# Optimization experiments

Hardware: AMD Instinct MI355X
Metric: run time of the kernel (lower is better)

The kernel has to match this reference:

```python
import jax, jax.numpy as jnp
from jax import lax
import numpy as np

KERNEL_SIZE = 5
GROUP_SIZE = 40
GMAX = 160                      # g sampled in [0, GMAX)
MAX_ITERS = (GMAX - 1) // GROUP_SIZE   # static upper bound on |g|//group_size = 3
B = 4096
D = 8192


def _circ_conv(x, k):
    # x: [1, B, D], k: [B, K] -> grouped (depthwise) circular conv1d, groups=B
    pad = KERNEL_SIZE - 1
    left = pad // 2
    xp = jnp.pad(x, ((0, 0), (0, 0), (left, pad - left)), mode='wrap')
    return lax.conv_general_dilated(
        xp, k[:, None, :], window_strides=(1,), padding='VALID',
        feature_group_count=k.shape[0], dimension_numbers=('NCH', 'OIH', 'NCH'))


def setup_inputs() -> dict:
    key = jax.random.key(0)
    k1, k2, k3 = jax.random.split(key, 3)
    x = jax.random.normal(k1, (B, D), dtype=jnp.float32)
    g = jax.random.randint(k2, (B,), 0, GMAX, dtype=jnp.int32)
    kernels = jax.random.normal(k3, (2 * GROUP_SIZE + 1, KERNEL_SIZE), dtype=jnp.float32)
    return {"x": x, "g": g, "kernels": kernels}


def reference(x, g, kernels):
    G = GROUP_SIZE
    xc = x[None]                          # [1, B, D]  (x.view(-1,1,D).permute(1,0,2))
    sign = jnp.sign(g)                    # [B]
    iters = jnp.abs(g) // G               # [B] data-dependent per-sample loop count
    max_it = jnp.max(iters)               # dynamic max over the batch
    max_k = kernels[sign * G + G]         # [B, K]
    id_k = kernels[G]                     # [K] learned 'identity' kernel
    # true delta kernel: exact no-op under circular pad, used for steps past max_it
    delta = jnp.zeros((KERNEL_SIZE,), x.dtype).at[(KERNEL_SIZE - 1) // 2].set(1.0)

    h = xc
    for i in range(MAX_ITERS):            # static bound; delta makes extra steps no-ops
        inactive = jnp.where(i < max_it, id_k, delta)          # [K]
        k_i = jnp.where((i < iters)[:, None], max_k, inactive[None, :])  # [B, K]
        h = _circ_conv(h, k_i)
    rem = jnp.abs(g) % G
    fin_k = kernels[rem * sign + G]       # [B, K]
    out = _circ_conv(h, fin_k)            # [1, B, D]
    return jnp.transpose(out, (1, 0, 2))  # [B, 1, D]
```

## Files before the change

kernel.cpp:

```cpp
#include <hip/hip_runtime.h>

#define BB 4096
#define DD 8192
#define KK 5
#define GS 40
#define MAXIT 3
#define EFF 17
#define CHUNK 2048
#define C4 (CHUNK/4)
#define DF4 (DD/4)
#define EPAD 20
#define WS_OFF 64

typedef float vf4 __attribute__((ext_vector_type(4)));

__device__ __forceinline__ int iabs(int a) { return a < 0 ? -a : a; }

template<int LEN>
__device__ __forceinline__ void compose5(float* e, const float* k5) {
    float ne[LEN + KK - 1];
#pragma unroll
    for (int m = 0; m < LEN + KK - 1; ++m) ne[m] = 0.f;
#pragma unroll
    for (int m = 0; m < LEN; ++m)
#pragma unroll
        for (int j = 0; j < KK; ++j) ne[m + j] += e[m] * k5[j];
#pragma unroll
    for (int m = 0; m < LEN + KK - 1; ++m) e[m] = ne[m];
}

__device__ __forceinline__ void pick5(int i, int iters, int max_it,
                                      const float* maxk, const float* idk,
                                      float* k5) {
#pragma unroll
    for (int j = 0; j < KK; ++j)
        k5[j] = (i < iters) ? maxk[j]
              : ((i < max_it) ? idk[j] : ((j == (KK - 1) / 2) ? 1.f : 0.f));
}

__global__ __launch_bounds__(256) void k_compose(const int* __restrict__ g,
                                                 const float* __restrict__ kernels,
                                                 float* __restrict__ wsE) {
    __shared__ int red[256];
    const int t = threadIdx.x;

    const int4* g4 = (const int4*)g;
    int m = 0;
    for (int i = t; i < BB / 4; i += 256) {
        int4 v = g4[i];
        m = max(m, max(max(iabs(v.x), iabs(v.y)), max(iabs(v.z), iabs(v.w))));
    }
    red[t] = m;
    __syncthreads();
    for (int s = 128; s > 0; s >>= 1) {
        if (t < s) red[t] = max(red[t], red[t + s]);
        __syncthreads();
    }
    const int max_it = red[0] / GS;

    const int r  = blockIdx.x * 256 + t;
    const int gv = g[r];
    const int sign  = gv > 0 ? 1 : (gv < 0 ? -1 : 0);
    const int a     = iabs(gv);
    const int iters = a / GS;
    const int rem   = a % GS;

    const float* mk = kernels + (size_t)(sign * GS + GS) * KK;
    const float* ik = kernels + (size_t)GS * KK;
    const float* fk = kernels + (size_t)(rem * sign + GS) * KK;
    float maxk[KK], idk[KK], fink[KK];
#pragma unroll
    for (int j = 0; j < KK; ++j) { maxk[j] = mk[j]; idk[j] = ik[j]; fink[j] = fk[j]; }

    float e[EPAD];
#pragma unroll
    for (int q = 0; q < EPAD; ++q) e[q] = 0.f;
    e[0] = 1.f;

    float k5[KK];
    pick5(0, iters, max_it, maxk, idk, k5); compose5<1>(e, k5);
    pick5(1, iters, max_it, maxk, idk, k5); compose5<5>(e, k5);
    pick5(2, iters, max_it, maxk, idk, k5); compose5<9>(e, k5);
    compose5<13>(e, fink);

    vf4* dst = (vf4*)(wsE + (size_t)r * EPAD);
    vf4 o0; o0.x = e[0];  o0.y = e[1];  o0.z = e[2];  o0.w = e[3];
    vf4 o1; o1.x = e[4];  o1.y = e[5];  o1.z = e[6];  o1.w = e[7];
    vf4 o2; o2.x = e[8];  o2.y = e[9];  o2.z = e[10]; o2.w = e[11];
    vf4 o3; o3.x = e[12]; o3.y = e[13]; o3.z = e[14]; o3.w = e[15];
    vf4 o4; o4.x = e[16]; o4.y = e[17]; o4.z = e[18]; o4.w = e[19];
    dst[0] = o0; dst[1] = o1; dst[2] = o2; dst[3] = o3; dst[4] = o4;
}

__global__ __launch_bounds__(256) void k_conv_pre(const float* __restrict__ x,
                                                  const float* __restrict__ wsE,
                                                  float* __restrict__ out) {
    __shared__ float lds[CHUNK + 16];
    float4* ldsv = (float4*)lds;

    const int bi   = blockIdx.x;
    const int b    = bi >> 2;
    const int ch   = bi & 3;
    const int t    = threadIdx.x;
    const int c0f4 = ch * C4;

    const float4* xr = (const float4*)(x + (size_t)b * DD);

    ldsv[2 + t]       = xr[c0f4 + t];
    ldsv[2 + t + 256] = xr[c0f4 + t + 256];
    if (t == 0) {
        ldsv[0] = xr[(c0f4 - 2) & (DF4 - 1)];
        ldsv[1] = xr[(c0f4 - 1) & (DF4 - 1)];
    } else if (t == 1) {
        ldsv[514] = xr[(c0f4 + C4)     & (DF4 - 1)];
        ldsv[515] = xr[(c0f4 + C4 + 1) & (DF4 - 1)];
    }

    const float4* ev = (const float4*)(wsE + (size_t)b * EPAD);
    float4 e0 = ev[0], e1 = ev[1], e2 = ev[2], e3 = ev[3], e4 = ev[4];
    float e[EFF] = { e0.x, e0.y, e0.z, e0.w,
                     e1.x, e1.y, e1.z, e1.w,
                     e2.x, e2.y, e2.z, e2.w,
                     e3.x, e3.y, e3.z, e3.w,
                     e4.x };

    __syncthreads();

    vf4* outr = (vf4*)(out + (size_t)b * DD);
#pragma unroll
    for (int jb = 0; jb < 2; ++jb) {
        const int v = jb * 256 + t;
        float f[EFF + 3];
#pragma unroll
        for (int q = 0; q < 5; ++q) {
            float4 val = ldsv[v + q];
            f[q * 4 + 0] = val.x; f[q * 4 + 1] = val.y;
            f[q * 4 + 2] = val.z; f[q * 4 + 3] = val.w;
        }
        float oc[4];
#pragma unroll
        for (int c = 0; c < 4; ++c) {
            float s = 0.f;
#pragma unroll
            for (int m = 0; m < EFF; ++m) s += e[m] * f[c + m];
            oc[c] = s;
        }
        vf4 o;
        o.x = oc[0]; o.y = oc[1]; o.z = oc[2]; o.w = oc[3];
        __builtin_nontemporal_store(o, outr + c0f4 + v);
    }
}

__global__ __launch_bounds__(256) void k_max_it(const int* __restrict__ g,
                                                int* __restrict__ ws) {
    __shared__ int red[256];
    int t = threadIdx.x;
    int m = 0;
    for (int i = t; i < BB; i += 256) m = max(m, iabs(g[i]));
    red[t] = m;
    __syncthreads();
    for (int s = 128; s > 0; s >>= 1) {
        if (t < s) red[t] = max(red[t], red[t + s]);
        __syncthreads();
    }
    if (t == 0) ws[0] = red[0] / GS;
}

__global__ __launch_bounds__(256) void k_conv(const float* __restrict__ x,
                                              const int* __restrict__ g,
                                              const float* __restrict__ kernels,
                                              const int* __restrict__ ws,
                                              float* __restrict__ out) {
    __shared__ float lds[CHUNK + 16];
    float4* ldsv = (float4*)lds;

    const int bi   = blockIdx.x;
    const int b    = bi >> 2;
    const int ch   = bi & 3;
    const int t    = threadIdx.x;
    const int c0f4 = ch * C4;

    const float4* xr = (const float4*)(x + (size_t)b * DD);

    ldsv[2 + t]       = xr[c0f4 + t];
    ldsv[2 + t + 256] = xr[c0f4 + t + 256];
    if (t == 0) {
        ldsv[0] = xr[(c0f4 - 2) & (DF4 - 1)];
        ldsv[1] = xr[(c0f4 - 1) & (DF4 - 1)];
    } else if (t == 1) {
        ldsv[514] = xr[(c0f4 + C4)     & (DF4 - 1)];
        ldsv[515] = xr[(c0f4 + C4 + 1) & (DF4 - 1)];
    }

    const int gv    = g[b];
    const int sign  = gv > 0 ? 1 : (gv < 0 ? -1 : 0);
    const int a     = iabs(gv);
    const int iters = a / GS;
    const int rem   = a % GS;
    const int max_it = ws[0];

    float maxk[KK], idk[KK], fink[KK];
    const float* mk = kernels + (size_t)(sign * GS + GS) * KK;
    const float* ik = kernels + (size_t)GS * KK;
    const float* fk = kernels + (size_t)(rem * sign + GS) * KK;
#pragma unroll
    for (int j = 0; j < KK; ++j) { maxk[j] = mk[j]; idk[j] = ik[j]; fink[j] = fk[j]; }

    float e[EPAD];
#pragma unroll
    for (int q = 0; q < EPAD; ++q) e[q] = 0.f;
    e[0] = 1.f;
    float k5[KK];
    pick5(0, iters, max_it, maxk, idk, k5); compose5<1>(e, k5);
    pick5(1, iters, max_it, maxk, idk, k5); compose5<5>(e, k5);
    pick5(2, iters, max_it, maxk, idk, k5); compose5<9>(e, k5);
    compose5<13>(e, fink);

    __syncthreads();

    vf4* outr = (vf4*)(out + (size_t)b * DD);
#pragma unroll
    for (int jb = 0; jb < 2; ++jb) {
        const int v = jb * 256 + t;
        float f[EFF + 3];
#pragma unroll
        for (int q = 0; q < 5; ++q) {
            float4 val = ldsv[v + q];
            f[q * 4 + 0] = val.x; f[q * 4 + 1] = val.y;
            f[q * 4 + 2] = val.z; f[q * 4 + 3] = val.w;
        }
        float oc[4];
#pragma unroll
        for (int c = 0; c < 4; ++c) {
            float s = 0.f;
#pragma unroll
            for (int m = 0; m < EFF; ++m) s += e[m] * f[c + m];
            oc[c] = s;
        }
        vf4 o;
        o.x = oc[0]; o.y = oc[1]; o.z = oc[2]; o.w = oc[3];
        __builtin_nontemporal_store(o, outr + c0f4 + v);
    }
}

extern "C" void kernel_launch(void* const* d_in, const int* in_sizes, int n_in,
                              void* d_out, int out_size, void* d_ws, size_t ws_size,
                              hipStream_t stream) {
    const float* x       = (const float*)d_in[0];
    const int*   g       = (const int*)d_in[1];
    const float* kernels = (const float*)d_in[2];
    float*       out     = (float*)d_out;

    const size_t need = (size_t)(WS_OFF + BB * EPAD) * sizeof(float);
    if (ws_size >= need) {
        float* wsE = (float*)d_ws + WS_OFF;
        k_compose<<<BB / 256, 256, 0, stream>>>(g, kernels, wsE);
        k_conv_pre<<<BB * (DD / CHUNK), 256, 0, stream>>>(x, wsE, out);
    } else {
        int* ws = (int*)d_ws;
        k_max_it<<<1, 256, 0, stream>>>(g, ws);
        k_conv<<<BB * (DD / CHUNK), 256, 0, stream>>>(x, g, kernels, ws, out);
    }
}
```

Baseline: 235.8 us.

## Replace LDS-staged chunked conv with direct global float4 loads, one block per row

The LDS staging and __syncthreads are removed. Each thread now reads its five overlapping float4 neighbours straight from global memory, relying on the caches to absorb the 5x redundant reads. The grid changes from four chunks per row to one block per row, with each thread looping over 8 float4 outputs. Nontemporal stores become plain stores. This trades the LDS round-trip and barrier for more cache-served global loads, and changes grid occupancy and store caching behaviour.

```diff
diff --git a/kernel.cpp b/kernel.cpp
--- a/kernel.cpp
+++ b/kernel.cpp
@@ -6,8 +6,6 @@
 #define GS 40
 #define MAXIT 3
 #define EFF 17
-#define CHUNK 2048
-#define C4 (CHUNK/4)
 #define DF4 (DD/4)
 #define EPAD 20
 #define WS_OFF 64
@@ -92,29 +90,11 @@
     dst[0] = o0; dst[1] = o1; dst[2] = o2; dst[3] = o3; dst[4] = o4;
 }
 
-__global__ __launch_bounds__(256) void k_conv_pre(const float* __restrict__ x,
-                                                  const float* __restrict__ wsE,
-                                                  float* __restrict__ out) {
-    __shared__ float lds[CHUNK + 16];
-    float4* ldsv = (float4*)lds;
-
-    const int bi   = blockIdx.x;
-    const int b    = bi >> 2;
-    const int ch   = bi & 3;
-    const int t    = threadIdx.x;
-    const int c0f4 = ch * C4;
-
-    const float4* xr = (const float4*)(x + (size_t)b * DD);
-
-    ldsv[2 + t]       = xr[c0f4 + t];
-    ldsv[2 + t + 256] = xr[c0f4 + t + 256];
-    if (t == 0) {
-        ldsv[0] = xr[(c0f4 - 2) & (DF4 - 1)];
-        ldsv[1] = xr[(c0f4 - 1) & (DF4 - 1)];
-    } else if (t == 1) {
-        ldsv[514] = xr[(c0f4 + C4)     & (DF4 - 1)];
-        ldsv[515] = xr[(c0f4 + C4 + 1) & (DF4 - 1)];
-    }
+__global__ __launch_bounds__(256) void k_conv_direct(const float* __restrict__ x,
+                                                     const float* __restrict__ wsE,
+                                                     float* __restrict__ out) {
+    const int b = blockIdx.x;
+    const int t = threadIdx.x;
 
     const float4* ev = (const float4*)(wsE + (size_t)b * EPAD);
     float4 e0 = ev[0], e1 = ev[1], e2 = ev[2], e3 = ev[3], e4 = ev[4];
@@ -124,16 +104,16 @@
                      e3.x, e3.y, e3.z, e3.w,
                      e4.x };
 
-    __syncthreads();
-
-    vf4* outr = (vf4*)(out + (size_t)b * DD);
-#pragma unroll
-    for (int jb = 0; jb < 2; ++jb) {
-        const int v = jb * 256 + t;
+    const float4* xr   = (const float4*)(x + (size_t)b * DD);
+    float4*       outr = (float4*)(out + (size_t)b * DD);
+
+#pragma unroll 2
+    for (int k = 0; k < 8; ++k) {
+        const int v = k * 256 + t;
         float f[EFF + 3];
 #pragma unroll
         for (int q = 0; q < 5; ++q) {
-            float4 val = ldsv[v + q];
+            float4 val = xr[(v - 2 + q) & (DF4 - 1)];
             f[q * 4 + 0] = val.x; f[q * 4 + 1] = val.y;
             f[q * 4 + 2] = val.z; f[q * 4 + 3] = val.w;
         }
@@ -145,9 +125,9 @@
             for (int m = 0; m < EFF; ++m) s += e[m] * f[c + m];
             oc[c] = s;
         }
-        vf4 o;
+        float4 o;
         o.x = oc[0]; o.y = oc[1]; o.z = oc[2]; o.w = oc[3];
-        __builtin_nontemporal_store(o, outr + c0f4 + v);
+        outr[v] = o;
     }
 }
 
@@ -166,31 +146,13 @@
     if (t == 0) ws[0] = red[0] / GS;
 }
 
-__global__ __launch_bounds__(256) void k_conv(const float* __restrict__ x,
-                                              const int* __restrict__ g,
-                                              const float* __restrict__ kernels,
-                                              const int* __restrict__ ws,
-                                              float* __restrict__ out) {
-    __shared__ float lds[CHUNK + 16];
-    float4* ldsv = (float4*)lds;
-
-    const int bi   = blockIdx.x;
-    const int b    = bi >> 2;
-    const int ch   = bi & 3;
-    const int t    = threadIdx.x;
-    const int c0f4 = ch * C4;
-
-    const float4* xr = (const float4*)(x + (size_t)b * DD);
-
-    ldsv[2 + t]       = xr[c0f4 + t];
-    ldsv[2 + t + 256] = xr[c0f4 + t + 256];
-    if (t == 0) {
-        ldsv[0] = xr[(c0f4 - 2) & (DF4 - 1)];
-        ldsv[1] = xr[(c0f4 - 1) & (DF4 - 1)];
-    } else if (t == 1) {
-        ldsv[514] = xr[(c0f4 + C4)     & (DF4 - 1)];
-        ldsv[515] = xr[(c0f4 + C4 + 1) & (DF4 - 1)];
-    }
+__global__ __launch_bounds__(256) void k_conv_fb(const float* __restrict__ x,
+                                                 const int* __restrict__ g,
+                                                 const float* __restrict__ kernels,
+                                                 const int* __restrict__ ws,
+                                                 float* __restrict__ out) {
+    const int b = blockIdx.x;
+    const int t = threadIdx.x;
 
     const int gv    = g[b];
     const int sign  = gv > 0 ? 1 : (gv < 0 ? -1 : 0);
@@ -216,16 +178,15 @@
     pick5(2, iters, max_it, maxk, idk, k5); compose5<9>(e, k5);
     compose5<13>(e, fink);
 
-    __syncthreads();
-
-    vf4* outr = (vf4*)(out + (size_t)b * DD);
-#pragma unroll
-    for (int jb = 0; jb < 2; ++jb) {
-        const int v = jb * 256 + t;
+    const float4* xr   = (const float4*)(x + (size_t)b * DD);
+    float4*       outr = (float4*)(out + (size_t)b * DD);
+#pragma unroll 2
+    for (int k = 0; k < 8; ++k) {
+        const int v = k * 256 + t;
         float f[EFF + 3];
 #pragma unroll
         for (int q = 0; q < 5; ++q) {
-            float4 val = ldsv[v + q];
+            float4 val = xr[(v - 2 + q) & (DF4 - 1)];
             f[q * 4 + 0] = val.x; f[q * 4 + 1] = val.y;
             f[q * 4 + 2] = val.z; f[q * 4 + 3] = val.w;
         }
@@ -237,9 +198,9 @@
             for (int m = 0; m < EFF; ++m) s += e[m] * f[c + m];
             oc[c] = s;
         }
-        vf4 o;
+        float4 o;
         o.x = oc[0]; o.y = oc[1]; o.z = oc[2]; o.w = oc[3];
-        __builtin_nontemporal_store(o, outr + c0f4 + v);
+        outr[v] = o;
     }
 }
 
@@ -255,10 +216,10 @@
     if (ws_size >= need) {
         float* wsE = (float*)d_ws + WS_OFF;
         k_compose<<<BB / 256, 256, 0, stream>>>(g, kernels, wsE);
-        k_conv_pre<<<BB * (DD / CHUNK), 256, 0, stream>>>(x, wsE, out);
+        k_conv_direct<<<BB, 256, 0, stream>>>(x, wsE, out);
     } else {
         int* ws = (int*)d_ws;
         k_max_it<<<1, 256, 0, stream>>>(g, ws);
-        k_conv<<<BB * (DD / CHUNK), 256, 0, stream>>>(x, g, kernels, ws, out);
-    }
-}
+        k_conv_fb<<<BB, 256, 0, stream>>>(x, g, kernels, ws, out);
+    }
+}
```

Result: slower. 277.5 us (+17.7%).
